# Kernel tuning notes

Measured on AMD Instinct MI355X. Metric: run time of the kernel, lower is better.

Reference implementation:

```python
import jax, jax.numpy as jnp
import numpy as np

EMB_DIM = 1024
N_HEADS = 16
HEAD_DIM = EMB_DIM // N_HEADS
WINDOW = 128
B, T = 4, 2048


def setup_inputs() -> dict:
    key = jax.random.key(0)
    k1, k2, k3 = jax.random.split(key, 3)
    x = jax.random.normal(k1, (B, T, EMB_DIM), dtype=jnp.float32)
    # nn.Linear weights: stored as [out, in], applied as x @ W^T
    s1 = 1.0 / np.sqrt(EMB_DIM)
    w_qkv = jax.random.uniform(k2, (3 * EMB_DIM, EMB_DIM), jnp.float32, -s1, s1)
    w_out = jax.random.uniform(k3, (EMB_DIM, EMB_DIM), jnp.float32, -s1, s1)
    return {"x": x, "w_qkv": w_qkv, "w_out": w_out}


def reference(x, w_qkv, w_out):
    Bs, Ts, C = x.shape
    scale = HEAD_DIM ** -0.5
    qkv = x @ w_qkv.T                                   # [B,T,3C]
    qkv = qkv.reshape(Bs, Ts, 3, N_HEADS, HEAD_DIM)
    qkv = jnp.transpose(qkv, (2, 0, 3, 1, 4))           # [3,B,H,T,D]
    q, k, v = qkv[0], qkv[1], qkv[2]
    scores = jnp.einsum('bhtd,bhsd->bhts', q, k) * scale  # [B,H,T,T]
    i = jnp.arange(Ts)[:, None]
    j = jnp.arange(Ts)[None, :]
    # causal AND within sliding window: i - WINDOW <= j <= i
    allowed = (j <= i) & (j >= i - WINDOW)               # [T,T] bool
    scores = jnp.where(allowed[None, None], scores, -jnp.inf)
    attn = jax.nn.softmax(scores, axis=-1)
    out = jnp.einsum('bhts,bhsd->bhtd', attn, v)         # [B,H,T,D]
    out = jnp.transpose(out, (0, 2, 1, 3)).reshape(Bs, Ts, C)
    return out @ w_out.T
```

## Files before the change

kernel.cpp:

```cpp
#include <hip/hip_runtime.h>
#include <hip/hip_bf16.h>
#include <stdint.h>

typedef __attribute__((ext_vector_type(8))) short bf16x8;
typedef __attribute__((ext_vector_type(4))) float f32x4;
typedef __attribute__((ext_vector_type(4))) unsigned short u16x4;

#define B_ 4
#define T_ 2048
#define C_ 1024
#define H_ 16
#define D_ 64

__device__ __forceinline__ unsigned short f2bf(float f) {
  union { float f; uint32_t u; } v; v.f = f;
  uint32_t u = v.u;
  uint32_t r = (u + 0x7FFFu + ((u >> 16) & 1u)) >> 16;
  return (unsigned short)r;
}

__global__ void __launch_bounds__(256) cast_f32_bf16(const float* __restrict__ src,
                                                     unsigned short* __restrict__ dst,
                                                     int n4) {
  int i = blockIdx.x * 256 + threadIdx.x;
  if (i >= n4) return;
  float4 f = ((const float4*)src)[i];
  u16x4 o;
  o[0] = f2bf(f.x); o[1] = f2bf(f.y); o[2] = f2bf(f.z); o[3] = f2bf(f.w);
  ((u16x4*)dst)[i] = o;
}

template <int MODE>
__global__ void __launch_bounds__(256) gemm_bt(const unsigned short* __restrict__ A,
                                               const unsigned short* __restrict__ Bm,
                                               unsigned short* __restrict__ qb,
                                               unsigned short* __restrict__ kb,
                                               unsigned short* __restrict__ vb,
                                               float* __restrict__ fo) {
  __shared__ short lds[16896];
  const int tid = threadIdx.x;

  const int nwgx = gridDim.x;
  int flat = blockIdx.y * nwgx + blockIdx.x;
  int cpx = (nwgx << 6) >> 3;
  int swz = (flat & 7) * cpx + (flat >> 3);
  const int bm = (swz & 63) * 128;
  const int bn = (swz >> 6) * 128;

  const int wave = tid >> 6;
  const int l = tid & 63;
  const int wm = wave >> 1, wn = wave & 1;
  const int lm = l & 15, lq = l >> 4;
  const int lr = l >> 2;
  const int lc = (l & 3) << 3;

  f32x4 acc[4][4];
#pragma unroll
  for (int i = 0; i < 4; i++)
#pragma unroll
    for (int j = 0; j < 4; j++) acc[i][j] = (f32x4){0.f, 0.f, 0.f, 0.f};

  const unsigned short* gsrc[4];
  int ldoff[4];
#pragma unroll
  for (int i = 0; i < 4; i++) {
    int c = wave * 4 + i;
    if (c < 8) {
      gsrc[i] = A + (size_t)(bm + 16 * c + lr) * 1024 + lc;
      ldoff[i] = (16 * c) * 32;
    } else {
      gsrc[i] = Bm + (size_t)(bn + 16 * (c - 8) + lr) * 1024 + lc;
      ldoff[i] = 8192 + (16 * (c - 8)) * 32;
    }
  }

#define STAGE(curb, kk)                                                          \
  do {                                                                           \
    _Pragma("unroll")                                                            \
    for (int i = 0; i < 4; i++) {                                                \
      __builtin_amdgcn_global_load_lds(                                          \
          (__attribute__((address_space(1))) void*)(uintptr_t)(const void*)(gsrc[i] + (kk)), \
          (__attribute__((address_space(3))) void*)(lds + ldoff[i] + (curb) * 4096),         \
          16, 0, 0);                                                             \
    }                                                                            \
  } while (0)

  STAGE(0, 0);
  int cur = 0;
  __syncthreads();

  for (int k0 = 0; k0 < 1024; k0 += 32) {
    if (k0 + 32 < 1024) STAGE(cur ^ 1, k0 + 32);
    bf16x8 af[4], bfr[4];
#pragma unroll
    for (int i = 0; i < 4; i++)
      af[i] = *(const bf16x8*)&lds[cur * 4096 + (wm * 64 + 16 * i + lm) * 32 + 8 * lq];
#pragma unroll
    for (int j = 0; j < 4; j++)
      bfr[j] = *(const bf16x8*)&lds[8192 + cur * 4096 + (wn * 64 + 16 * j + lm) * 32 + 8 * lq];
#pragma unroll
    for (int i = 0; i < 4; i++)
#pragma unroll
      for (int j = 0; j < 4; j++)
        acc[i][j] = __builtin_amdgcn_mfma_f32_16x16x32_bf16(af[i], bfr[j], acc[i][j], 0, 0, 0);
    __syncthreads();
    cur ^= 1;
  }
#undef STAGE

  if (MODE == 0) {
#pragma unroll
    for (int i = 0; i < 4; i++)
#pragma unroll
      for (int j = 0; j < 4; j++)
#pragma unroll
        for (int r = 0; r < 4; r++)
          lds[(wm * 64 + 16 * i + 4 * lq + r) * 132 + wn * 64 + 16 * j + lm] =
              (short)f2bf(acc[i][j][r]);
    __syncthreads();
#pragma unroll
    for (int k = 0; k < 8; k++) {
      int c = tid + 256 * k;
      int row = c >> 4;
      int col = (c & 15) << 3;
      bf16x8 v = *(const bf16x8*)&lds[row * 132 + col];
      int m = bm + row, n = bn + col;
      int which = n >> 10, rem = n & 1023;
      int h = rem >> 6, d = rem & 63;
      int b = m >> 11, t = m & 2047;
      unsigned short* dst = (which == 0) ? qb : ((which == 1) ? kb : vb);
      *(bf16x8*)&dst[(((size_t)(b * 16 + h)) * 2048 + t) * 64 + d] = v;
    }
  } else {
#pragma unroll
    for (int i = 0; i < 4; i++)
#pragma unroll
      for (int j = 0; j < 4; j++)
#pragma unroll
        for (int r = 0; r < 4; r++) {
          int m = bm + wm * 64 + 16 * i + 4 * lq + r;
          int n = bn + wn * 64 + 16 * j + lm;
          fo[(size_t)m * 1024 + n] = acc[i][j][r];
        }
  }
}

__global__ void __launch_bounds__(256) attn_swa(const unsigned short* __restrict__ Qb,
                                               const unsigned short* __restrict__ Kb,
                                               const unsigned short* __restrict__ Vb,
                                               unsigned short* __restrict__ Ob) {
  __shared__ short P[4][16 * 40];
  const int wv = threadIdx.x >> 6;
  const int l = threadIdx.x & 63;
  const int wid = blockIdx.x * 4 + wv;
  const int bh = wid >> 7;
  const int t0 = (wid & 127) << 4;
  const int lm = l & 15, lq = l >> 4;
  const size_t base = (size_t)bh * (T_ * D_);

  bf16x8 aq0 = *(const bf16x8*)(Qb + base + (size_t)(t0 + lm) * 64 + 8 * lq);
  bf16x8 aq1 = *(const bf16x8*)(Qb + base + (size_t)(t0 + lm) * 64 + 32 + 8 * lq);

  float mst[4], lst[4];
  f32x4 Oa[4];
#pragma unroll
  for (int r = 0; r < 4; r++) { mst[r] = -1e30f; lst[r] = 0.f; }
#pragma unroll
  for (int jt = 0; jt < 4; jt++) Oa[jt] = (f32x4){0.f, 0.f, 0.f, 0.f};

  const float cs = 0.125f * 1.44269504f;
  int jstart = t0 - 128; if (jstart < 0) jstart = 0;

  for (int j0 = jstart; j0 < t0 + 16; j0 += 32) {
    f32x4 S[2];
#pragma unroll
    for (int hh = 0; hh < 2; hh++) {
      int kr = j0 + 16 * hh + lm; if (kr > T_ - 1) kr = T_ - 1;
      bf16x8 bk0 = *(const bf16x8*)(Kb + base + (size_t)kr * 64 + 8 * lq);
      bf16x8 bk1 = *(const bf16x8*)(Kb + base + (size_t)kr * 64 + 32 + 8 * lq);
      f32x4 s = (f32x4){0.f, 0.f, 0.f, 0.f};
      s = __builtin_amdgcn_mfma_f32_16x16x32_bf16(aq0, bk0, s, 0, 0, 0);
      s = __builtin_amdgcn_mfma_f32_16x16x32_bf16(aq1, bk1, s, 0, 0, 0);
      S[hh] = s;
    }
    float p0s[4], p1s[4], al[4];
#pragma unroll
    for (int r = 0; r < 4; r++) {
      int t = t0 + 4 * lq + r;
      int ja = j0 + lm, jb = j0 + 16 + lm;
      float s0 = ((ja <= t) && (ja + 128 >= t)) ? S[0][r] * cs : -1e30f;
      float s1 = ((jb <= t) && (jb + 128 >= t)) ? S[1][r] * cs : -1e30f;
      float m2 = fmaxf(s0, s1);
#pragma unroll
      for (int off = 1; off < 16; off <<= 1) m2 = fmaxf(m2, __shfl_xor(m2, off));
      float mn = fmaxf(mst[r], m2);
      float a = __builtin_amdgcn_exp2f(mst[r] - mn);
      float p0 = __builtin_amdgcn_exp2f(s0 - mn);
      float p1 = __builtin_amdgcn_exp2f(s1 - mn);
      float ps = p0 + p1;
#pragma unroll
      for (int off = 1; off < 16; off <<= 1) ps += __shfl_xor(ps, off);
      lst[r] = lst[r] * a + ps;
      mst[r] = mn;
      al[r] = a; p0s[r] = p0; p1s[r] = p1;
    }
#pragma unroll
    for (int jt = 0; jt < 4; jt++)
#pragma unroll
      for (int r = 0; r < 4; r++) Oa[jt][r] *= al[r];
#pragma unroll
    for (int r = 0; r < 4; r++) {
      P[wv][(4 * lq + r) * 40 + lm] = (short)f2bf(p0s[r]);
      P[wv][(4 * lq + r) * 40 + 16 + lm] = (short)f2bf(p1s[r]);
    }
    bf16x8 pa = *(const bf16x8*)&P[wv][lm * 40 + 8 * lq];
#pragma unroll
    for (int jt = 0; jt < 4; jt++) {
      bf16x8 vf;
#pragma unroll
      for (int jj = 0; jj < 8; jj++) {
        int kk = j0 + 8 * lq + jj; if (kk > T_ - 1) kk = T_ - 1;
        vf[jj] = (short)Vb[base + (size_t)kk * 64 + 16 * jt + lm];
      }
      Oa[jt] = __builtin_amdgcn_mfma_f32_16x16x32_bf16(pa, vf, Oa[jt], 0, 0, 0);
    }
  }
  const int b = bh >> 4, h = bh & 15;
#pragma unroll
  for (int r = 0; r < 4; r++) {
    float inv = 1.0f / lst[r];
    int t = t0 + 4 * lq + r;
#pragma unroll
    for (int jt = 0; jt < 4; jt++) {
      int c = h * 64 + 16 * jt + lm;
      Ob[((size_t)(b * T_ + t)) * 1024 + c] = f2bf(Oa[jt][r] * inv);
    }
  }
}

extern "C" void kernel_launch(void* const* d_in, const int* in_sizes, int n_in,
                              void* d_out, int out_size, void* d_ws, size_t ws_size,
                              hipStream_t stream) {
  const float* x = (const float*)d_in[0];
  const float* w_qkv = (const float*)d_in[1];
  const float* w_out = (const float*)d_in[2];
  float* out = (float*)d_out;

  unsigned short* xb = (unsigned short*)d_ws;
  unsigned short* wqkvb = xb + (size_t)8192 * 1024;
  unsigned short* woutb = wqkvb + (size_t)3072 * 1024;
  unsigned short* qb = woutb + (size_t)1024 * 1024;
  unsigned short* kb = qb + (size_t)64 * 2048 * 64;
  unsigned short* vb = kb + (size_t)64 * 2048 * 64;

  cast_f32_bf16<<<8192, 256, 0, stream>>>(x, xb, 8192 * 1024 / 4);
  cast_f32_bf16<<<3072, 256, 0, stream>>>(w_qkv, wqkvb, 3072 * 1024 / 4);
  cast_f32_bf16<<<1024, 256, 0, stream>>>(w_out, woutb, 1024 * 1024 / 4);

  gemm_bt<0><<<dim3(24, 64), 256, 0, stream>>>(xb, wqkvb, qb, kb, vb, nullptr);

  attn_swa<<<2048, 256, 0, stream>>>(qb, kb, vb, xb);

  gemm_bt<1><<<dim3(8, 64), 256, 0, stream>>>(xb, woutb, nullptr, nullptr, nullptr, out);
}
```

Baseline: 219.4 us.

## Rewrite QKV GEMM with 256x256 tiles, direct global-to-LDS loads, 4-stage pipeline

```diff
diff --git a/kernel.cpp b/kernel.cpp
--- a/kernel.cpp
+++ b/kernel.cpp
@@ -30,23 +30,145 @@
   ((u16x4*)dst)[i] = o;
 }
 
-template <int MODE>
-__global__ void __launch_bounds__(256) gemm_bt(const unsigned short* __restrict__ A,
-                                               const unsigned short* __restrict__ Bm,
-                                               unsigned short* __restrict__ qb,
-                                               unsigned short* __restrict__ kb,
-                                               unsigned short* __restrict__ vb,
-                                               float* __restrict__ fo) {
-  __shared__ short lds[16896];
+__global__ void __launch_bounds__(512, 2) gemm_qkv256(const unsigned short* __restrict__ A,
+                                                      const unsigned short* __restrict__ Bm,
+                                                      unsigned short* __restrict__ qb,
+                                                      unsigned short* __restrict__ kb,
+                                                      unsigned short* __restrict__ vb) {
+  __shared__ short lds[65536];
   const int tid = threadIdx.x;
-
-  const int nwgx = gridDim.x;
-  int flat = blockIdx.y * nwgx + blockIdx.x;
-  int cpx = (nwgx << 6) >> 3;
-  int swz = (flat & 7) * cpx + (flat >> 3);
-  const int bm = (swz & 63) * 128;
-  const int bn = (swz >> 6) * 128;
-
+  const int bm = blockIdx.y * 256;
+  const int bn = blockIdx.x * 256;
+  const int wave = tid >> 6;
+  const int l = tid & 63;
+  const int wr = wave >> 2;
+  const int wc = wave & 3;
+  const int lm = l & 15, lq = l >> 4;
+
+  f32x4 acc[8][4];
+#pragma unroll
+  for (int i = 0; i < 8; i++)
+#pragma unroll
+    for (int j = 0; j < 4; j++) acc[i][j] = (f32x4){0.f, 0.f, 0.f, 0.f};
+
+  const unsigned short* gs[4];
+  int ldo[4];
+#pragma unroll
+  for (int i = 0; i < 4; i++) {
+    int c = i * 512 + tid;
+    if (c < 1024) {
+      int row = c >> 2, kc = c & 3;
+      gs[i] = A + (size_t)(bm + row) * 1024 + kc * 8;
+      ldo[i] = c * 8;
+    } else {
+      int cb = c - 1024;
+      int row = cb >> 2, kc = cb & 3;
+      gs[i] = Bm + (size_t)(bn + row) * 1024 + kc * 8;
+      ldo[i] = 32768 + cb * 8;
+    }
+  }
+
+#define G2L(i, t)                                                                 \
+  __builtin_amdgcn_global_load_lds(                                               \
+      (__attribute__((address_space(1))) void*)(uintptr_t)(const void*)(gs[i] + (t) * 32), \
+      (__attribute__((address_space(3))) void*)(lds + ldo[i] + ((t) & 3) * 8192), \
+      16, 0, 0)
+#define FENCE() __builtin_amdgcn_sched_barrier(0)
+
+#pragma unroll
+  for (int t = 0; t < 3; t++) {
+    G2L(0, t); G2L(1, t); G2L(2, t); G2L(3, t);
+  }
+  FENCE();
+  asm volatile("s_waitcnt vmcnt(8)" ::: "memory");
+  __builtin_amdgcn_s_barrier();
+  FENCE();
+
+  for (int t = 0; t < 32; ++t) {
+    const int s = t & 3;
+    const short* As_ = lds + s * 8192;
+    const short* Bs_ = lds + 32768 + s * 8192;
+    bf16x8 Af[4], Bf[4];
+    if (t + 3 < 32) { G2L(0, t + 3); G2L(1, t + 3); }
+#pragma unroll
+    for (int i = 0; i < 4; i++)
+      Af[i] = *(const bf16x8*)&As_[(wr * 128 + 16 * i + lm) * 32 + 8 * lq];
+#pragma unroll
+    for (int j = 0; j < 4; j++)
+      Bf[j] = *(const bf16x8*)&Bs_[(wc * 64 + 16 * j + lm) * 32 + 8 * lq];
+    FENCE();
+    __builtin_amdgcn_s_barrier();
+    FENCE();
+    __builtin_amdgcn_s_setprio(1);
+#pragma unroll
+    for (int i = 0; i < 4; i++)
+#pragma unroll
+      for (int j = 0; j < 4; j++)
+        acc[i][j] = __builtin_amdgcn_mfma_f32_16x16x32_bf16(Af[i], Bf[j], acc[i][j], 0, 0, 0);
+    __builtin_amdgcn_s_setprio(0);
+    FENCE();
+    __builtin_amdgcn_s_barrier();
+    FENCE();
+    if (t + 3 < 32) { G2L(2, t + 3); G2L(3, t + 3); }
+#pragma unroll
+    for (int i = 0; i < 4; i++)
+      Af[i] = *(const bf16x8*)&As_[(wr * 128 + 64 + 16 * i + lm) * 32 + 8 * lq];
+    FENCE();
+    __builtin_amdgcn_s_barrier();
+    FENCE();
+    __builtin_amdgcn_s_setprio(1);
+#pragma unroll
+    for (int i = 0; i < 4; i++)
+#pragma unroll
+      for (int j = 0; j < 4; j++)
+        acc[4 + i][j] = __builtin_amdgcn_mfma_f32_16x16x32_bf16(Af[i], Bf[j], acc[4 + i][j], 0, 0, 0);
+    __builtin_amdgcn_s_setprio(0);
+    FENCE();
+    if (t < 29) asm volatile("s_waitcnt vmcnt(8)" ::: "memory");
+    else        asm volatile("s_waitcnt vmcnt(0)" ::: "memory");
+    __builtin_amdgcn_s_barrier();
+    FENCE();
+  }
+#undef G2L
+
+#pragma unroll
+  for (int p = 0; p < 2; ++p) {
+    if (p) __syncthreads();
+    if (wr == p) {
+#pragma unroll
+      for (int i = 0; i < 8; i++)
+#pragma unroll
+        for (int j = 0; j < 4; j++)
+#pragma unroll
+          for (int r = 0; r < 4; r++)
+            lds[(16 * i + 4 * lq + r) * 264 + wc * 64 + 16 * j + lm] =
+                (short)f2bf(acc[i][j][r]);
+    }
+    __syncthreads();
+#pragma unroll
+    for (int k = 0; k < 8; k++) {
+      int c = tid + 512 * k;
+      int row = c >> 5;
+      int col = (c & 31) << 3;
+      bf16x8 v = *(const bf16x8*)&lds[row * 264 + col];
+      int m = bm + p * 128 + row;
+      int n = bn + col;
+      int which = n >> 10, rem = n & 1023;
+      int h = rem >> 6, d = rem & 63;
+      int b = m >> 11, t = m & 2047;
+      unsigned short* dst = (which == 0) ? qb : ((which == 1) ? kb : vb);
+      *(bf16x8*)&dst[(((size_t)(b * 16 + h)) * 2048 + t) * 64 + d] = v;
+    }
+  }
+}
+
+__global__ void __launch_bounds__(256) gemm_out(const unsigned short* __restrict__ A,
+                                                const unsigned short* __restrict__ Bm,
+                                                float* __restrict__ fo) {
+  __shared__ short lds[16384];
+  const int tid = threadIdx.x;
+  const int bm = blockIdx.y * 128;
+  const int bn = blockIdx.x * 128;
   const int wave = tid >> 6;
   const int l = tid & 63;
   const int wm = wave >> 1, wn = wave & 1;
@@ -108,41 +230,16 @@
   }
 #undef STAGE
 
-  if (MODE == 0) {
-#pragma unroll
-    for (int i = 0; i < 4; i++)
-#pragma unroll
-      for (int j = 0; j < 4; j++)
-#pragma unroll
-        for (int r = 0; r < 4; r++)
-          lds[(wm * 64 + 16 * i + 4 * lq + r) * 132 + wn * 64 + 16 * j + lm] =
-              (short)f2bf(acc[i][j][r]);
-    __syncthreads();
-#pragma unroll
-    for (int k = 0; k < 8; k++) {
-      int c = tid + 256 * k;
-      int row = c >> 4;
-      int col = (c & 15) << 3;
-      bf16x8 v = *(const bf16x8*)&lds[row * 132 + col];
-      int m = bm + row, n = bn + col;
-      int which = n >> 10, rem = n & 1023;
-      int h = rem >> 6, d = rem & 63;
-      int b = m >> 11, t = m & 2047;
-      unsigned short* dst = (which == 0) ? qb : ((which == 1) ? kb : vb);
-      *(bf16x8*)&dst[(((size_t)(b * 16 + h)) * 2048 + t) * 64 + d] = v;
-    }
-  } else {
-#pragma unroll
-    for (int i = 0; i < 4; i++)
-#pragma unroll
-      for (int j = 0; j < 4; j++)
-#pragma unroll
-        for (int r = 0; r < 4; r++) {
-          int m = bm + wm * 64 + 16 * i + 4 * lq + r;
-          int n = bn + wn * 64 + 16 * j + lm;
-          fo[(size_t)m * 1024 + n] = acc[i][j][r];
-        }
-  }
+#pragma unroll
+  for (int i = 0; i < 4; i++)
+#pragma unroll
+    for (int j = 0; j < 4; j++)
+#pragma unroll
+      for (int r = 0; r < 4; r++) {
+        int m = bm + wm * 64 + 16 * i + 4 * lq + r;
+        int n = bn + wn * 64 + 16 * j + lm;
+        fo[(size_t)m * 1024 + n] = acc[i][j][r];
+      }
 }
 
 __global__ void __launch_bounds__(256) attn_swa(const unsigned short* __restrict__ Qb,
@@ -257,9 +354,9 @@
   cast_f32_bf16<<<3072, 256, 0, stream>>>(w_qkv, wqkvb, 3072 * 1024 / 4);
   cast_f32_bf16<<<1024, 256, 0, stream>>>(w_out, woutb, 1024 * 1024 / 4);
 
-  gemm_bt<0><<<dim3(24, 64), 256, 0, stream>>>(xb, wqkvb, qb, kb, vb, nullptr);
+  gemm_qkv256<<<dim3(12, 32), 512, 0, stream>>>(xb, wqkvb, qb, kb, vb);
 
   attn_swa<<<2048, 256, 0, stream>>>(qb, kb, vb, xb);
 
-  gemm_bt<1><<<dim3(8, 64), 256, 0, stream>>>(xb, woutb, nullptr, nullptr, nullptr, out);
-}
+  gemm_out<<<dim3(8, 64), 256, 0, stream>>>(xb, woutb, out);
+}
```

Measured after the change: 233.2 us. 6.3% more time.

## Store V transposed from QKV GEMM so attention loads V fragments vectorized

Applied to the files above, without the earlier changes.

```diff
diff --git a/kernel.cpp b/kernel.cpp
--- a/kernel.cpp
+++ b/kernel.cpp
@@ -39,13 +39,8 @@
                                                float* __restrict__ fo) {
   __shared__ short lds[16896];
   const int tid = threadIdx.x;
-
-  const int nwgx = gridDim.x;
-  int flat = blockIdx.y * nwgx + blockIdx.x;
-  int cpx = (nwgx << 6) >> 3;
-  int swz = (flat & 7) * cpx + (flat >> 3);
-  const int bm = (swz & 63) * 128;
-  const int bn = (swz >> 6) * 128;
+  const int bm = blockIdx.y * 128;
+  const int bn = blockIdx.x * 128;
 
   const int wave = tid >> 6;
   const int l = tid & 63;
@@ -109,27 +104,43 @@
 #undef STAGE
 
   if (MODE == 0) {
-#pragma unroll
-    for (int i = 0; i < 4; i++)
-#pragma unroll
-      for (int j = 0; j < 4; j++)
-#pragma unroll
-        for (int r = 0; r < 4; r++)
-          lds[(wm * 64 + 16 * i + 4 * lq + r) * 132 + wn * 64 + 16 * j + lm] =
-              (short)f2bf(acc[i][j][r]);
-    __syncthreads();
-#pragma unroll
-    for (int k = 0; k < 8; k++) {
-      int c = tid + 256 * k;
-      int row = c >> 4;
-      int col = (c & 15) << 3;
-      bf16x8 v = *(const bf16x8*)&lds[row * 132 + col];
-      int m = bm + row, n = bn + col;
-      int which = n >> 10, rem = n & 1023;
-      int h = rem >> 6, d = rem & 63;
-      int b = m >> 11, t = m & 2047;
-      unsigned short* dst = (which == 0) ? qb : ((which == 1) ? kb : vb);
-      *(bf16x8*)&dst[(((size_t)(b * 16 + h)) * 2048 + t) * 64 + d] = v;
+    if (bn >= 2048) {
+#pragma unroll
+      for (int i = 0; i < 4; i++)
+#pragma unroll
+        for (int j = 0; j < 4; j++) {
+          int m0 = bm + wm * 64 + 16 * i + 4 * lq;
+          int n = (bn - 2048) + wn * 64 + 16 * j + lm;
+          int h = n >> 6, d = n & 63;
+          int b = m0 >> 11, t = m0 & 2047;
+          u16x4 o;
+#pragma unroll
+          for (int r = 0; r < 4; r++) o[r] = f2bf(acc[i][j][r]);
+          *(u16x4*)&vb[(((size_t)(b * 16 + h)) * 64 + d) * 2048 + t] = o;
+        }
+    } else {
+#pragma unroll
+      for (int i = 0; i < 4; i++)
+#pragma unroll
+        for (int j = 0; j < 4; j++)
+#pragma unroll
+          for (int r = 0; r < 4; r++)
+            lds[(wm * 64 + 16 * i + 4 * lq + r) * 132 + wn * 64 + 16 * j + lm] =
+                (short)f2bf(acc[i][j][r]);
+      __syncthreads();
+#pragma unroll
+      for (int k = 0; k < 8; k++) {
+        int c = tid + 256 * k;
+        int row = c >> 4;
+        int col = (c & 15) << 3;
+        bf16x8 v = *(const bf16x8*)&lds[row * 132 + col];
+        int m = bm + row, n = bn + col;
+        int which = n >> 10, rem = n & 1023;
+        int h = rem >> 6, d = rem & 63;
+        int b = m >> 11, t = m & 2047;
+        unsigned short* dst = (which == 0) ? qb : kb;
+        *(bf16x8*)&dst[(((size_t)(b * 16 + h)) * 2048 + t) * 64 + d] = v;
+      }
     }
   } else {
 #pragma unroll
@@ -147,7 +158,7 @@
 
 __global__ void __launch_bounds__(256) attn_swa(const unsigned short* __restrict__ Qb,
                                                const unsigned short* __restrict__ Kb,
-                                               const unsigned short* __restrict__ Vb,
+                                               const unsigned short* __restrict__ Vt,
                                                unsigned short* __restrict__ Ob) {
   __shared__ short P[4][16 * 40];
   const int wv = threadIdx.x >> 6;
@@ -216,12 +227,7 @@
     bf16x8 pa = *(const bf16x8*)&P[wv][lm * 40 + 8 * lq];
 #pragma unroll
     for (int jt = 0; jt < 4; jt++) {
-      bf16x8 vf;
-#pragma unroll
-      for (int jj = 0; jj < 8; jj++) {
-        int kk = j0 + 8 * lq + jj; if (kk > T_ - 1) kk = T_ - 1;
-        vf[jj] = (short)Vb[base + (size_t)kk * 64 + 16 * jt + lm];
-      }
+      bf16x8 vf = *(const bf16x8*)(Vt + base + (size_t)(16 * jt + lm) * 2048 + j0 + 8 * lq);
       Oa[jt] = __builtin_amdgcn_mfma_f32_16x16x32_bf16(pa, vf, Oa[jt], 0, 0, 0);
     }
   }
```

Result: slower. 229.7 us (+4.7%).
